# Performance work log

Measured on AMD Instinct MI355X. Metric: run time of the kernel, lower is better.

The kernel has to match this reference:

```python
import jax, jax.numpy as jnp
import numpy as np

MARGIN = 0.3  # init_kwargs
EPS = 1e-12   # torch F.normalize eps


def _pairwise_dist(f):
    # Euclidean cdist via the stable quadratic expansion; f is [B, D].
    sq = jnp.sum(f * f, axis=1)                      # [B]
    d2 = sq[:, None] + sq[None, :] - 2.0 * (f @ f.T)  # [B, B]
    d2 = jnp.maximum(d2, 0.0)
    # safe sqrt: zero distance (diagonal / duplicates) -> 0 with zero grad
    pos = d2 > 0.0
    return jnp.sqrt(jnp.where(pos, d2, 1.0)) * pos


def reference(features, labels):
    B = features.shape[0]
    norm = jnp.linalg.norm(features, axis=1, keepdims=True)
    f = features / jnp.maximum(norm, EPS)            # F.normalize(dim=1)

    dist = _pairwise_dist(f)                         # [B, B]
    mask = labels[:, None] == labels[None, :]        # positives (incl. self)

    pos_count = jnp.sum(mask, axis=1)                # [B], >= 1 (self)
    has_pos = pos_count > 1                          # needs another positive
    has_neg = pos_count < B                          # at least one negative
    valid = has_pos & has_neg

    # mean over positive distances (includes the self-distance 0, as in torch code)
    mean_pos = jnp.sum(dist * mask, axis=1) / pos_count.astype(dist.dtype)  # [B]

    # semi-hard negatives: negatives with dist > mean positive dist
    sh_mask = (~mask) & (dist > mean_pos[:, None])   # [B, B]
    has_sh = jnp.any(sh_mask, axis=1)
    min_sh = jnp.min(jnp.where(sh_mask, dist, jnp.inf), axis=1)
    min_sh = jnp.where(has_sh, min_sh, 0.0)          # guard inf for invalid rows

    contrib = valid & has_sh
    per_anchor = jax.nn.relu(mean_pos - min_sh + MARGIN)
    loss_sum = jnp.sum(jnp.where(contrib, per_anchor, 0.0))
    count = jnp.sum(contrib)
    return jnp.where(count > 0, loss_sum / count.astype(dist.dtype), 0.0)


def setup_inputs() -> dict:
    key = jax.random.key(0)
    k1, k2 = jax.random.split(key)
    features = jax.random.normal(k1, (8192, 512), dtype=jnp.float32)
    labels = jax.random.randint(k2, (8192,), 0, 128, dtype=jnp.int64)
    return {"features": features, "labels": labels}
```

## Files before the change

kernel.cpp:

```cpp
#include <hip/hip_runtime.h>
#include <math.h>

#define EPS_N 1e-12f
#define MARGIN 0.3f
#define INF_BITS 0x7f800000u
#define NCLS 128
#define D 512
#define PADR 256

typedef __attribute__((ext_vector_type(8))) short short8;
typedef __attribute__((ext_vector_type(4))) float float4v;

__device__ __forceinline__ unsigned short f2bf(float f) {
    unsigned u = __float_as_uint(f);
    u += 0x7fff + ((u >> 16) & 1);
    return (unsigned short)(u >> 16);
}
__device__ __forceinline__ void gl16(const void* g, void* l) {
    __builtin_amdgcn_global_load_lds((const __attribute__((address_space(1))) void*)g,
                                     (__attribute__((address_space(3))) void*)l, 16, 0, 0);
}

__global__ __launch_bounds__(1024) void k_bucket(const int* __restrict__ lab, int Bn,
        int* __restrict__ pos, int* __restrict__ labp,
        int* __restrict__ cstart_g, int* __restrict__ ccnt_g,
        float* __restrict__ meanpos, float* __restrict__ pcinv,
        int* __restrict__ poscnt, unsigned* __restrict__ minbits) {
    __shared__ int cnt[NCLS], off[NCLS], sa[NCLS], sb[NCLS];
    int tid = threadIdx.x;
    if (tid < NCLS) cnt[tid] = 0;
    __syncthreads();
    for (int i = tid; i < Bn; i += 1024) atomicAdd(&cnt[lab[i] & (NCLS - 1)], 1);
    __syncthreads();
    if (tid < NCLS) sa[tid] = cnt[tid];
    __syncthreads();
    int* src = sa; int* dst = sb;
    for (int ofs = 1; ofs < NCLS; ofs <<= 1) {
        if (tid < NCLS) dst[tid] = src[tid] + ((tid >= ofs) ? src[tid - ofs] : 0);
        __syncthreads();
        int* t = src; src = dst; dst = t;
    }
    if (tid < NCLS) {
        int ex = src[tid] - cnt[tid];
        off[tid] = ex;
        cstart_g[tid] = ex;
        ccnt_g[tid] = cnt[tid];
    }
    __syncthreads();
    for (int i = tid; i < Bn; i += 1024) {
        int l = lab[i] & (NCLS - 1);
        int p = atomicAdd(&off[l], 1);
        int m = cnt[l];
        pos[i] = p;
        labp[p] = l;
        poscnt[p] = m;
        pcinv[p] = 1.0f / (float)m;
        meanpos[p] = 0.f;
        minbits[p] = INF_BITS;
    }
}

__global__ __launch_bounds__(256) void k_normalize(const float* __restrict__ x,
        const int* __restrict__ pos, unsigned short* __restrict__ fh,
        float* __restrict__ sqp) {
    int w = threadIdx.x >> 6, L = threadIdx.x & 63;
    int row = blockIdx.x * 4 + w;
    const float* xr = x + (size_t)row * D + L * 8;
    float4 a = *(const float4*)xr;
    float4 b = *(const float4*)(xr + 4);
    float ss = a.x * a.x;
    ss = fmaf(a.y, a.y, ss); ss = fmaf(a.z, a.z, ss); ss = fmaf(a.w, a.w, ss);
    ss = fmaf(b.x, b.x, ss); ss = fmaf(b.y, b.y, ss);
    ss = fmaf(b.z, b.z, ss); ss = fmaf(b.w, b.w, ss);
    #pragma unroll
    for (int off = 32; off; off >>= 1) ss += __shfl_xor(ss, off, 64);
    float inv = 1.0f / fmaxf(sqrtf(ss), EPS_N);
    int prow = pos[row];
    if (L == 0) sqp[prow] = ss * inv * inv;
    ushort4 h0, h1;
    h0.x = f2bf(a.x * inv); h0.y = f2bf(a.y * inv);
    h0.z = f2bf(a.z * inv); h0.w = f2bf(a.w * inv);
    h1.x = f2bf(b.x * inv); h1.y = f2bf(b.y * inv);
    h1.z = f2bf(b.z * inv); h1.w = f2bf(b.w * inv);
    unsigned short* dst = fh + (size_t)prow * D + L * 8;
    *(ushort4*)dst = h0;
    *(ushort4*)(dst + 4) = h1;
}

__global__ __launch_bounds__(256) void k_posband3(
    const unsigned short* __restrict__ fh, const float* __restrict__ sqp,
    const int* __restrict__ labp, const int* __restrict__ cstart_g,
    const int* __restrict__ ccnt_g, float* __restrict__ meanpos, int Bn)
{
    __shared__ unsigned short SA[16 * 128];
    __shared__ unsigned short SB[128 * 128];
    __shared__ float sqr[16], rs[16];
    __shared__ int labr[16];
    __shared__ float sqc[128];
    __shared__ int labc[128];

    const int r0 = blockIdx.x * 16;
    const int tid = threadIdx.x, w = tid >> 6, L = tid & 63;
    const int lm = L & 15, ls = L >> 4;
    const int srow = L >> 4;
    const int sseg = L & 15;

    if (tid < 16) {
        labr[tid] = labp[r0 + tid];
        sqr[tid]  = sqp[r0 + tid];
        rs[tid]   = 0.f;
    }
    __syncthreads();
    const int c0 = cstart_g[labr[0]];
    const int c1 = cstart_g[labr[15]] + ccnt_g[labr[15]];

    for (int cc0 = c0; cc0 < c1; cc0 += 128) {
        __syncthreads();
        if (tid < 128) {
            int q = cc0 + tid;
            if (q < Bn) { sqc[tid] = sqp[q]; labc[tid] = labp[q]; }
            else        { sqc[tid] = 0.f;    labc[tid] = -1; }
        }
        float4v acc[2];
        acc[0] = (float4v){0.f, 0.f, 0.f, 0.f};
        acc[1] = (float4v){0.f, 0.f, 0.f, 0.f};

        for (int k0 = 0; k0 < D; k0 += 128) {
            __syncthreads();
            {
                int rmat = w * 4 + srow;
                int seg = sseg ^ (rmat & 15);
                gl16(fh + (size_t)(r0 + rmat) * D + k0 + seg * 8, &SA[(w * 4) * 128]);
            }
            #pragma unroll
            for (int it = 0; it < 8; ++it) {
                int rmat = it * 16 + w * 4 + srow;
                int seg = sseg ^ (rmat & 15);
                gl16(fh + (size_t)(cc0 + rmat) * D + k0 + seg * 8,
                     &SB[(size_t)(it * 16 + w * 4) * 128]);
            }
            __syncthreads();
            #pragma unroll
            for (int h = 0; h < 4; ++h) {
                int ra = lm;
                short8 af = *(const short8*)&SA[ra * 128 + (((h * 4 + ls) ^ (ra & 15))) * 8];
                #pragma unroll
                for (int ct = 0; ct < 2; ++ct) {
                    int rb = w * 32 + ct * 16 + lm;
                    short8 bf = *(const short8*)&SB[rb * 128 + (((h * 4 + ls) ^ (rb & 15))) * 8];
                    acc[ct] = __builtin_amdgcn_mfma_f32_16x16x32_bf16(af, bf, acc[ct], 0, 0, 0);
                }
            }
        }
        #pragma unroll
        for (int v = 0; v < 4; ++v) {
            int ri = ls * 4 + v;
            int p = r0 + ri;
            int lr = labr[ri];
            float sr = sqr[ri];
            float sum = 0.f;
            #pragma unroll
            for (int ct = 0; ct < 2; ++ct) {
                int ci = w * 32 + ct * 16 + lm;
                int q = cc0 + ci;
                float d2 = sr + sqc[ci] - 2.0f * acc[ct][v];
                float dd = (d2 > 0.f) ? sqrtf(d2) : 0.f;
                sum += ((labc[ci] == lr) && (q != p)) ? dd : 0.f;
            }
            #pragma unroll
            for (int off = 8; off; off >>= 1) sum += __shfl_xor(sum, off, 64);
            if (lm == 0) atomicAdd(&rs[ri], sum);
        }
    }
    __syncthreads();
    if (tid < 16 && rs[tid] != 0.f) atomicAdd(&meanpos[r0 + tid], rs[tid]);
}

#define BKG 64

__global__ __launch_bounds__(256, 4) void k_minsh_mfma(
    const unsigned short* __restrict__ fh, const float* __restrict__ sqp,
    const int* __restrict__ labp, const float* __restrict__ meanpos,
    const float* __restrict__ pcinv, unsigned* __restrict__ minbits)
{
    int t = blockIdx.x;
    int rq = (int)((sqrtf(8.0f * (float)t + 1.0f) - 1.0f) * 0.5f);
    while ((rq + 1) * (rq + 2) / 2 <= t) ++rq;
    while (rq * (rq + 1) / 2 > t) --rq;
    int cq = t - rq * (rq + 1) / 2;
    const int i0 = cq * 128, j0 = rq * 128;
    const bool diag = (i0 == j0);

    __shared__ unsigned short LA[2][128 * BKG];
    __shared__ float s_mp2r[128], s_mp2c[128], s_sqr[128], s_sqc[128];
    __shared__ int s_labr[128], s_labc[128];

    const int tid = threadIdx.x;
    const int w = tid >> 6, L = tid & 63;

    if (tid < 128) {
        float mp = meanpos[i0 + tid] * pcinv[i0 + tid];
        s_mp2r[tid] = mp * mp;
        s_sqr[tid]  = sqp[i0 + tid];
        s_labr[tid] = labp[i0 + tid];
    } else {
        int q = tid - 128;
        float mp = meanpos[j0 + q] * pcinv[j0 + q];
        s_mp2c[q] = mp * mp;
        s_sqc[q]  = sqp[j0 + q];
        s_labc[q] = labp[j0 + q];
    }

    const unsigned short* msrc = fh + (size_t)((w < 2) ? i0 : j0) * D;
    unsigned short* mylds = &LA[(w < 2) ? 0 : 1][(w & 1) * 64 * BKG];
    const int srow = L >> 3;
    const int sseg = L & 7;

    float4v acc[4][4];
    #pragma unroll
    for (int a = 0; a < 4; ++a)
        #pragma unroll
        for (int b = 0; b < 4; ++b) acc[a][b] = (float4v){0.f, 0.f, 0.f, 0.f};

    const int rw = (w >> 1) * 64, cw = (w & 1) * 64;
    const int lm = L & 15, ls = L >> 4;

    for (int k0 = 0; k0 < D; k0 += BKG) {
        __syncthreads();
        #pragma unroll
        for (int it = 0; it < 8; ++it) {
            int rmat = (w & 1) * 64 + it * 8 + srow;
            int seg = sseg ^ (rmat & 7);
            gl16(msrc + (size_t)rmat * D + k0 + seg * 8, mylds + it * 512);
        }
        __syncthreads();
        #pragma unroll
        for (int h = 0; h < 2; ++h) {
            short8 ah[4], bh[4];
            #pragma unroll
            for (int mi = 0; mi < 4; ++mi) {
                int r = rw + mi * 16 + lm;
                int slot = r * 8 + ((h * 4 + ls) ^ (r & 7));
                ah[mi] = *(const short8*)&LA[0][slot * 8];
            }
            #pragma unroll
            for (int ni = 0; ni < 4; ++ni) {
                int cc = cw + ni * 16 + lm;
                int slot = cc * 8 + ((h * 4 + ls) ^ (cc & 7));
                bh[ni] = *(const short8*)&LA[1][slot * 8];
            }
            #pragma unroll
            for (int ni = 0; ni < 4; ++ni)
                #pragma unroll
                for (int mi = 0; mi < 4; ++mi)
                    acc[mi][ni] = __builtin_amdgcn_mfma_f32_16x16x32_bf16(ah[mi], bh[ni], acc[mi][ni], 0, 0, 0);
        }
    }

    const float INFF = __uint_as_float(INF_BITS);
    float sc[4], mp2c[4];
    int lc[4];
    #pragma unroll
    for (int ni = 0; ni < 4; ++ni) {
        int cl = cw + ni * 16 + lm;
        sc[ni]   = s_sqc[cl];
        mp2c[ni] = s_mp2c[cl];
        lc[ni]   = s_labc[cl];
    }
    float vminc[4];
    #pragma unroll
    for (int ni = 0; ni < 4; ++ni) vminc[ni] = INFF;

    #pragma unroll
    for (int mi = 0; mi < 4; ++mi) {
        #pragma unroll
        for (int v = 0; v < 4; ++v) {
            int rl = rw + mi * 16 + ls * 4 + v;
            float mp2r = s_mp2r[rl];
            float sr   = s_sqr[rl];
            int   li   = s_labr[rl];
            float vminr = INFF;
            #pragma unroll
            for (int ni = 0; ni < 4; ++ni) {
                float d2 = fmaf(-2.0f, acc[mi][ni][v], sr + sc[ni]);
                bool neq = (li != lc[ni]);
                vminr     = fminf(vminr,     (neq && d2 > mp2r)     ? d2 : INFF);
                vminc[ni] = fminf(vminc[ni], (neq && d2 > mp2c[ni]) ? d2 : INFF);
            }
            #pragma unroll
            for (int off = 8; off; off >>= 1)
                vminr = fminf(vminr, __shfl_xor(vminr, off, 64));
            if (lm == 0 && __float_as_uint(vminr) != INF_BITS)
                atomicMin(&minbits[i0 + rl], __float_as_uint(vminr));
        }
    }
    if (!diag) {
        #pragma unroll
        for (int ni = 0; ni < 4; ++ni) {
            float vc = vminc[ni];
            vc = fminf(vc, __shfl_xor(vc, 16, 64));
            vc = fminf(vc, __shfl_xor(vc, 32, 64));
            if (ls == 0 && __float_as_uint(vc) != INF_BITS)
                atomicMin(&minbits[j0 + cw + ni * 16 + lm], __float_as_uint(vc));
        }
    }
}

__global__ __launch_bounds__(1024) void k_finish(const float* __restrict__ meanpos,
        const float* __restrict__ pcinv, const int* __restrict__ poscnt,
        const unsigned* __restrict__ minbits, float* __restrict__ out, int Bn) {
    float lsum = 0.f; int lcnt = 0;
    for (int i = threadIdx.x; i < Bn; i += 1024) {
        int pc = poscnt[i];
        bool valid = (pc > 1) && (pc < Bn);
        unsigned mb = minbits[i];
        if (valid && mb != INF_BITS) {
            float v = fmaf(meanpos[i], pcinv[i], MARGIN - sqrtf(__uint_as_float(mb)));
            lsum += (v > 0.f) ? v : 0.f;
            lcnt += 1;
        }
    }
    __shared__ float ssum[16]; __shared__ int scnt[16];
    int lane = threadIdx.x & 63, wid = threadIdx.x >> 6;
    #pragma unroll
    for (int off = 32; off; off >>= 1) {
        lsum += __shfl_down(lsum, off, 64);
        lcnt += __shfl_down(lcnt, off, 64);
    }
    if (lane == 0) { ssum[wid] = lsum; scnt[wid] = lcnt; }
    __syncthreads();
    if (threadIdx.x == 0) {
        float s = 0.f; int c = 0;
        #pragma unroll
        for (int q = 0; q < 16; ++q) { s += ssum[q]; c += scnt[q]; }
        out[0] = (c > 0) ? s / (float)c : 0.f;
    }
}

extern "C" void kernel_launch(void* const* d_in, const int* in_sizes, int n_in,
                              void* d_out, int out_size, void* d_ws, size_t ws_size,
                              hipStream_t stream) {
    const float* x = (const float*)d_in[0];
    const int* lab = (const int*)d_in[1];
    int Bn = in_sizes[1];

    size_t nd = (size_t)(Bn + PADR) * D;
    unsigned short* fh = (unsigned short*)d_ws;
    float* sqp        = (float*)(fh + nd);
    float* meanpos    = sqp + Bn;
    float* pcinv      = meanpos + Bn;
    int* poscnt       = (int*)(pcinv + Bn);
    unsigned* minbits = (unsigned*)(poscnt + Bn);
    int* pos          = (int*)(minbits + Bn);
    int* labp         = pos + Bn;
    int* cstart_g     = labp + Bn;
    int* ccnt_g       = cstart_g + NCLS;

    k_bucket<<<1, 1024, 0, stream>>>(lab, Bn, pos, labp, cstart_g, ccnt_g,
                                     meanpos, pcinv, poscnt, minbits);
    k_normalize<<<Bn / 4, 256, 0, stream>>>(x, pos, fh, sqp);
    k_posband3<<<Bn / 16, 256, 0, stream>>>(fh, sqp, labp, cstart_g, ccnt_g,
                                            meanpos, Bn);
    int nb = Bn / 128;
    int T = nb * (nb + 1) / 2;
    k_minsh_mfma<<<T, 256, 0, stream>>>(fh, sqp, labp, meanpos, pcinv, minbits);
    k_finish<<<1, 1024, 0, stream>>>(meanpos, pcinv, poscnt, minbits,
                                     (float*)d_out, Bn);
}
```

Measured before the change: 177.7 us.

## Fuse final reduction into last minsh block and remap tile order

Drops the separate k_finish launch: each k_minsh_mfma block bumps a global done counter, and the last block to finish computes the final loss. Block indices are remapped with an 8-way interleave (b&7)*(Tot/8)+(b>>3), which looks aimed at spreading tiles across XCDs for L2 locality. k_bucket now fills the per-position arrays by binary searching the class prefix sums instead of using the atomic scatter, leaving atomics only for pos. The fused tail relies on an atomic counter without an explicit memory fence, and the remap assumes Tot is divisible by 8.

```diff
diff --git a/kernel.cpp b/kernel.cpp
--- a/kernel.cpp
+++ b/kernel.cpp
@@ -25,9 +25,11 @@
         int* __restrict__ pos, int* __restrict__ labp,
         int* __restrict__ cstart_g, int* __restrict__ ccnt_g,
         float* __restrict__ meanpos, float* __restrict__ pcinv,
-        int* __restrict__ poscnt, unsigned* __restrict__ minbits) {
-    __shared__ int cnt[NCLS], off[NCLS], sa[NCLS], sb[NCLS];
+        int* __restrict__ poscnt, unsigned* __restrict__ minbits,
+        unsigned* __restrict__ done) {
+    __shared__ int cnt[NCLS], cs[NCLS + 1], off[NCLS], sa[NCLS], sb[NCLS];
     int tid = threadIdx.x;
+    if (tid == 0) done[0] = 0u;
     if (tid < NCLS) cnt[tid] = 0;
     __syncthreads();
     for (int i = tid; i < Bn; i += 1024) atomicAdd(&cnt[lab[i] & (NCLS - 1)], 1);
@@ -42,21 +44,30 @@
     }
     if (tid < NCLS) {
         int ex = src[tid] - cnt[tid];
+        cs[tid] = ex;
         off[tid] = ex;
         cstart_g[tid] = ex;
         ccnt_g[tid] = cnt[tid];
     }
-    __syncthreads();
-    for (int i = tid; i < Bn; i += 1024) {
-        int l = lab[i] & (NCLS - 1);
-        int p = atomicAdd(&off[l], 1);
-        int m = cnt[l];
-        pos[i] = p;
+    if (tid == 0) cs[NCLS] = Bn;
+    __syncthreads();
+    for (int p = tid; p < Bn; p += 1024) {
+        int lo = 0, hi = NCLS - 1;
+        #pragma unroll
+        for (int s = 0; s < 7; ++s) {
+            int mid = (lo + hi + 1) >> 1;
+            if (cs[mid] <= p) lo = mid; else hi = mid - 1;
+        }
+        int l = lo, m = cnt[l];
         labp[p] = l;
         poscnt[p] = m;
         pcinv[p] = 1.0f / (float)m;
         meanpos[p] = 0.f;
         minbits[p] = INF_BITS;
+    }
+    for (int i = tid; i < Bn; i += 1024) {
+        int l = lab[i] & (NCLS - 1);
+        pos[i] = atomicAdd(&off[l], 1);
     }
 }
 
@@ -181,9 +192,12 @@
 __global__ __launch_bounds__(256, 4) void k_minsh_mfma(
     const unsigned short* __restrict__ fh, const float* __restrict__ sqp,
     const int* __restrict__ labp, const float* __restrict__ meanpos,
-    const float* __restrict__ pcinv, unsigned* __restrict__ minbits)
+    const float* __restrict__ pcinv, const int* __restrict__ poscnt,
+    unsigned* __restrict__ minbits, unsigned* __restrict__ done,
+    float* __restrict__ out, int Bn, int Tot)
 {
-    int t = blockIdx.x;
+    int b = blockIdx.x;
+    int t = (b & 7) * (Tot >> 3) + (b >> 3);
     int rq = (int)((sqrtf(8.0f * (float)t + 1.0f) - 1.0f) * 0.5f);
     while ((rq + 1) * (rq + 2) / 2 <= t) ++rq;
     while (rq * (rq + 1) / 2 > t) --rq;
@@ -220,7 +234,7 @@
     #pragma unroll
     for (int a = 0; a < 4; ++a)
         #pragma unroll
-        for (int b = 0; b < 4; ++b) acc[a][b] = (float4v){0.f, 0.f, 0.f, 0.f};
+        for (int bq = 0; bq < 4; ++bq) acc[a][bq] = (float4v){0.f, 0.f, 0.f, 0.f};
 
     const int rw = (w >> 1) * 64, cw = (w & 1) * 64;
     const int lm = L & 15, ls = L >> 4;
@@ -304,36 +318,37 @@
                 atomicMin(&minbits[j0 + cw + ni * 16 + lm], __float_as_uint(vc));
         }
     }
-}
-
-__global__ __launch_bounds__(1024) void k_finish(const float* __restrict__ meanpos,
-        const float* __restrict__ pcinv, const int* __restrict__ poscnt,
-        const unsigned* __restrict__ minbits, float* __restrict__ out, int Bn) {
-    float lsum = 0.f; int lcnt = 0;
-    for (int i = threadIdx.x; i < Bn; i += 1024) {
-        int pc = poscnt[i];
-        bool valid = (pc > 1) && (pc < Bn);
-        unsigned mb = minbits[i];
-        if (valid && mb != INF_BITS) {
-            float v = fmaf(meanpos[i], pcinv[i], MARGIN - sqrtf(__uint_as_float(mb)));
-            lsum += (v > 0.f) ? v : 0.f;
-            lcnt += 1;
-        }
-    }
-    __shared__ float ssum[16]; __shared__ int scnt[16];
-    int lane = threadIdx.x & 63, wid = threadIdx.x >> 6;
-    #pragma unroll
-    for (int off = 32; off; off >>= 1) {
-        lsum += __shfl_down(lsum, off, 64);
-        lcnt += __shfl_down(lcnt, off, 64);
-    }
-    if (lane == 0) { ssum[wid] = lsum; scnt[wid] = lcnt; }
-    __syncthreads();
-    if (threadIdx.x == 0) {
-        float s = 0.f; int c = 0;
-        #pragma unroll
-        for (int q = 0; q < 16; ++q) { s += ssum[q]; c += scnt[q]; }
-        out[0] = (c > 0) ? s / (float)c : 0.f;
+
+    __shared__ int s_last;
+    __syncthreads();
+    if (tid == 0) s_last = (atomicAdd(done, 1u) == (unsigned)(Tot - 1)) ? 1 : 0;
+    __syncthreads();
+    if (s_last) {
+        float lsum = 0.f; int lcnt = 0;
+        for (int i = tid; i < Bn; i += 256) {
+            unsigned mb = atomicMin(&minbits[i], INF_BITS);
+            int pc = poscnt[i];
+            bool valid = (pc > 1) && (pc < Bn);
+            if (valid && mb != INF_BITS) {
+                float v = fmaf(meanpos[i], pcinv[i],
+                               MARGIN - sqrtf(__uint_as_float(mb)));
+                lsum += (v > 0.f) ? v : 0.f;
+                lcnt += 1;
+            }
+        }
+        __shared__ float ssum[4]; __shared__ int scnt[4];
+        #pragma unroll
+        for (int off = 32; off; off >>= 1) {
+            lsum += __shfl_down(lsum, off, 64);
+            lcnt += __shfl_down(lcnt, off, 64);
+        }
+        if (L == 0) { ssum[w] = lsum; scnt[w] = lcnt; }
+        __syncthreads();
+        if (tid == 0) {
+            float s = ssum[0] + ssum[1] + ssum[2] + ssum[3];
+            int   c = scnt[0] + scnt[1] + scnt[2] + scnt[3];
+            out[0] = (c > 0) ? s / (float)c : 0.f;
+        }
     }
 }
 
@@ -355,15 +370,15 @@
     int* labp         = pos + Bn;
     int* cstart_g     = labp + Bn;
     int* ccnt_g       = cstart_g + NCLS;
+    unsigned* done    = (unsigned*)(ccnt_g + NCLS);
 
     k_bucket<<<1, 1024, 0, stream>>>(lab, Bn, pos, labp, cstart_g, ccnt_g,
-                                     meanpos, pcinv, poscnt, minbits);
+                                     meanpos, pcinv, poscnt, minbits, done);
     k_normalize<<<Bn / 4, 256, 0, stream>>>(x, pos, fh, sqp);
     k_posband3<<<Bn / 16, 256, 0, stream>>>(fh, sqp, labp, cstart_g, ccnt_g,
                                             meanpos, Bn);
     int nb = Bn / 128;
     int T = nb * (nb + 1) / 2;
-    k_minsh_mfma<<<T, 256, 0, stream>>>(fh, sqp, labp, meanpos, pcinv, minbits);
-    k_finish<<<1, 1024, 0, stream>>>(meanpos, pcinv, poscnt, minbits,
-                                     (float*)d_out, Bn);
-}
+    k_minsh_mfma<<<T, 256, 0, stream>>>(fh, sqp, labp, meanpos, pcinv, poscnt,
+                                        minbits, done, (float*)d_out, Bn, T);
+}
```

Result: slower. 185.9 us (+4.6%).

## Fuse label bucketing into normalize kernel with per-row stable rank

Applied to the files above, without the earlier changes.

Removes the single-block bucketing kernel and merges it into the normalize kernel. Each of the 2048 blocks redundantly builds the 128-class histogram and prefix sum in shared memory, and each row computes its slot by counting earlier rows with the same label. This drops a serial one-block launch and the pos indirection buffer. In exchange every block rereads all labels, and each wave does O(row) work to compute its rank, which is quadratic in total.

```diff
diff --git a/kernel.cpp b/kernel.cpp
--- a/kernel.cpp
+++ b/kernel.cpp
@@ -21,16 +21,19 @@
                                      (__attribute__((address_space(3))) void*)l, 16, 0, 0);
 }
 
-__global__ __launch_bounds__(1024) void k_bucket(const int* __restrict__ lab, int Bn,
-        int* __restrict__ pos, int* __restrict__ labp,
-        int* __restrict__ cstart_g, int* __restrict__ ccnt_g,
-        float* __restrict__ meanpos, float* __restrict__ pcinv,
-        int* __restrict__ poscnt, unsigned* __restrict__ minbits) {
-    __shared__ int cnt[NCLS], off[NCLS], sa[NCLS], sb[NCLS];
-    int tid = threadIdx.x;
+__global__ __launch_bounds__(256) void k_normbucket(
+        const float* __restrict__ x, const int* __restrict__ lab, int Bn,
+        unsigned short* __restrict__ fh, float* __restrict__ sqp,
+        int* __restrict__ labp, float* __restrict__ meanpos,
+        float* __restrict__ pcinv, int* __restrict__ poscnt,
+        unsigned* __restrict__ minbits,
+        int* __restrict__ cstart_g, int* __restrict__ ccnt_g) {
+    __shared__ int cnt[NCLS], cs[NCLS], sa[NCLS], sb[NCLS];
+    int tid = threadIdx.x, w = tid >> 6, L = tid & 63;
+
     if (tid < NCLS) cnt[tid] = 0;
     __syncthreads();
-    for (int i = tid; i < Bn; i += 1024) atomicAdd(&cnt[lab[i] & (NCLS - 1)], 1);
+    for (int i = tid; i < Bn; i += 256) atomicAdd(&cnt[lab[i] & (NCLS - 1)], 1);
     __syncthreads();
     if (tid < NCLS) sa[tid] = cnt[tid];
     __syncthreads();
@@ -40,31 +43,17 @@
         __syncthreads();
         int* t = src; src = dst; dst = t;
     }
-    if (tid < NCLS) {
-        int ex = src[tid] - cnt[tid];
-        off[tid] = ex;
-        cstart_g[tid] = ex;
-        ccnt_g[tid] = cnt[tid];
-    }
-    __syncthreads();
-    for (int i = tid; i < Bn; i += 1024) {
-        int l = lab[i] & (NCLS - 1);
-        int p = atomicAdd(&off[l], 1);
-        int m = cnt[l];
-        pos[i] = p;
-        labp[p] = l;
-        poscnt[p] = m;
-        pcinv[p] = 1.0f / (float)m;
-        meanpos[p] = 0.f;
-        minbits[p] = INF_BITS;
-    }
-}
-
-__global__ __launch_bounds__(256) void k_normalize(const float* __restrict__ x,
-        const int* __restrict__ pos, unsigned short* __restrict__ fh,
-        float* __restrict__ sqp) {
-    int w = threadIdx.x >> 6, L = threadIdx.x & 63;
+    if (tid < NCLS) cs[tid] = src[tid] - cnt[tid];
+    __syncthreads();
+
     int row = blockIdx.x * 4 + w;
+    int mylab = lab[row] & (NCLS - 1);
+    int rk = 0;
+    for (int j = L; j < row; j += 64) rk += ((lab[j] & (NCLS - 1)) == mylab) ? 1 : 0;
+    #pragma unroll
+    for (int off = 32; off; off >>= 1) rk += __shfl_xor(rk, off, 64);
+    int prow = cs[mylab] + rk;
+
     const float* xr = x + (size_t)row * D + L * 8;
     float4 a = *(const float4*)xr;
     float4 b = *(const float4*)(xr + 4);
@@ -75,16 +64,28 @@
     #pragma unroll
     for (int off = 32; off; off >>= 1) ss += __shfl_xor(ss, off, 64);
     float inv = 1.0f / fmaxf(sqrtf(ss), EPS_N);
-    int prow = pos[row];
-    if (L == 0) sqp[prow] = ss * inv * inv;
+    if (L == 0) {
+        sqp[prow] = ss * inv * inv;
+        int m = cnt[mylab];
+        labp[prow] = mylab;
+        poscnt[prow] = m;
+        pcinv[prow] = 1.0f / (float)m;
+        meanpos[prow] = 0.f;
+        minbits[prow] = INF_BITS;
+    }
     ushort4 h0, h1;
     h0.x = f2bf(a.x * inv); h0.y = f2bf(a.y * inv);
     h0.z = f2bf(a.z * inv); h0.w = f2bf(a.w * inv);
     h1.x = f2bf(b.x * inv); h1.y = f2bf(b.y * inv);
     h1.z = f2bf(b.z * inv); h1.w = f2bf(b.w * inv);
-    unsigned short* dst = fh + (size_t)prow * D + L * 8;
-    *(ushort4*)dst = h0;
-    *(ushort4*)(dst + 4) = h1;
+    unsigned short* dst2 = fh + (size_t)prow * D + L * 8;
+    *(ushort4*)dst2 = h0;
+    *(ushort4*)(dst2 + 4) = h1;
+
+    if (blockIdx.x == 0 && tid < NCLS) {
+        cstart_g[tid] = cs[tid];
+        ccnt_g[tid] = cnt[tid];
+    }
 }
 
 __global__ __launch_bounds__(256) void k_posband3(
@@ -220,7 +221,7 @@
     #pragma unroll
     for (int a = 0; a < 4; ++a)
         #pragma unroll
-        for (int b = 0; b < 4; ++b) acc[a][b] = (float4v){0.f, 0.f, 0.f, 0.f};
+        for (int bq = 0; bq < 4; ++bq) acc[a][bq] = (float4v){0.f, 0.f, 0.f, 0.f};
 
     const int rw = (w >> 1) * 64, cw = (w & 1) * 64;
     const int lm = L & 15, ls = L >> 4;
@@ -351,14 +352,13 @@
     float* pcinv      = meanpos + Bn;
     int* poscnt       = (int*)(pcinv + Bn);
     unsigned* minbits = (unsigned*)(poscnt + Bn);
-    int* pos          = (int*)(minbits + Bn);
-    int* labp         = pos + Bn;
+    int* labp         = (int*)(minbits + Bn);
     int* cstart_g     = labp + Bn;
     int* ccnt_g       = cstart_g + NCLS;
 
-    k_bucket<<<1, 1024, 0, stream>>>(lab, Bn, pos, labp, cstart_g, ccnt_g,
-                                     meanpos, pcinv, poscnt, minbits);
-    k_normalize<<<Bn / 4, 256, 0, stream>>>(x, pos, fh, sqp);
+    k_normbucket<<<Bn / 4, 256, 0, stream>>>(x, lab, Bn, fh, sqp, labp, meanpos,
+                                             pcinv, poscnt, minbits,
+                                             cstart_g, ccnt_g);
     k_posband3<<<Bn / 16, 256, 0, stream>>>(fh, sqp, labp, cstart_g, ccnt_g,
                                             meanpos, Bn);
     int nb = Bn / 128;
```

New measurement: 171.4 us. -3.6%, faster.
